# Optimization experiments

Hardware: AMD Instinct MI355X
Metric: run time of the kernel (lower is better)

Reference implementation:

```python
import jax, jax.numpy as jnp
import numpy as np

B, S, D_MODEL, HEAD = 4, 4096, 1024, 64


def rope(x):
    # Faithful to the torch code: 'odd' = even-indexed elems, 'even' = odd-indexed.
    b, s, d = x.shape
    half = d // 2
    pos = jnp.arange(s, dtype=x.dtype)
    theta = 1.0 / (10000.0 ** (jnp.arange(half, dtype=x.dtype) / half))
    freqs = pos[:, None] * theta[None, :]  # (s, half)
    sin, cos = jnp.sin(freqs), jnp.cos(freqs)
    odd = x[..., 0::2]
    even = x[..., 1::2]
    x_rot_even = even * cos + odd * sin
    x_rot_odd = odd * cos - even * sin
    return jnp.stack([x_rot_odd, x_rot_even], axis=-1).reshape(x.shape)


def setup_inputs() -> dict:
    key = jax.random.key(0)
    kx, kq, kk, kv = jax.random.split(key, 4)
    x = jax.random.normal(kx, (B, S, D_MODEL), dtype=jnp.float32)
    # torch Linear weights are [out,in]; we store the transposed [in,out] form.
    sc = 1.0 / np.sqrt(D_MODEL)
    Wq = jax.random.normal(kq, (D_MODEL, HEAD), dtype=jnp.float32) * sc
    Wk = jax.random.normal(kk, (D_MODEL, HEAD), dtype=jnp.float32) * sc
    Wv = jax.random.normal(kv, (D_MODEL, HEAD), dtype=jnp.float32) * sc
    return {"x": x, "Wq": Wq, "Wk": Wk, "Wv": Wv}


def reference(x, Wq, Wk, Wv):
    Q = rope(x @ Wq)  # (B, S, H)
    K = rope(x @ Wk)
    V = x @ Wv
    scale = K.shape[-1] ** -0.5
    scores = jnp.einsum('bqh,bkh->bqk', Q, K) * scale  # (B, S, S)
    causal = jnp.tril(jnp.ones((S, S), dtype=bool))
    scores = jnp.where(causal, scores, -jnp.inf)
    probs = jax.nn.softmax(scores, axis=-1)  # dropout p treated as 0 (eval)
    return jnp.einsum('bqk,bkh->bqh', probs, V)
```

## Files before the change

### kernel.cpp

```cpp
#include <hip/hip_runtime.h>
#include <stdint.h>


static constexpr int S_LEN  = 4096;
static constexpr int DMODEL = 1024;
static constexpr int NS     = 6;
static constexpr float SHIFT2  = 11.541560327111707f;
static constexpr float QSCALE  = 0.18033688011112042f;

typedef __attribute__((ext_vector_type(8))) short bf16x8;
typedef __attribute__((ext_vector_type(4))) float f32x4;

#define MFMA16(a, b, c) __builtin_amdgcn_mfma_f32_16x16x32_bf16((a), (b), (c), 0, 0, 0)

__device__ __forceinline__ unsigned short f2b(float f) {
    union { float f; unsigned int u; } v;
    v.f = f;
    unsigned int u = v.u;
    u += 0x7fffu + ((u >> 16) & 1u);
    return (unsigned short)(u >> 16);
}
__device__ __forceinline__ float b2f(unsigned short b) {
    union { unsigned int u; float f; } v;
    v.u = ((unsigned int)b) << 16;
    return v.f;
}

__device__ __forceinline__ float fast_exp2(float x) {
#if __has_builtin(__builtin_amdgcn_exp2f)
    return __builtin_amdgcn_exp2f(x);
#else
    return exp2f(x);
#endif
}

template <int CTRL>
__device__ __forceinline__ float dpp_f(float v) {
    return __builtin_bit_cast(float,
        __builtin_amdgcn_update_dpp(0, __builtin_bit_cast(int, v), CTRL, 0xf, 0xf, false));
}
__device__ __forceinline__ float rowsum16(float v) {
    v += dpp_f<0x128>(v);
    v += dpp_f<0x124>(v);
    v += dpp_f<0x122>(v);
    v += dpp_f<0x121>(v);
    return v;
}

__device__ __forceinline__ void dma16(const void* g, void* l) {
    __builtin_amdgcn_global_load_lds(
        (const __attribute__((address_space(1))) unsigned int*)g,
        (__attribute__((address_space(3))) unsigned int*)l, 16, 0, 0);
}

__global__ __launch_bounds__(256) void prep_wt(const float* __restrict__ Wq,
                                               const float* __restrict__ Wk,
                                               const float* __restrict__ Wv,
                                               unsigned short* __restrict__ Wt) {
    int idx = blockIdx.x * 256 + threadIdx.x;
    int c = idx >> 10;
    int k = idx & 1023;
    int mat = c >> 6, n = c & 63;
    const float* W = (mat == 0) ? Wq : (mat == 1) ? Wk : Wv;
    Wt[idx] = f2b(W[k * 64 + n]);
}

__global__ __launch_bounds__(256, 2) void proj_rope(const float* __restrict__ x,
                                                    const unsigned short* __restrict__ Wt,
                                                    unsigned short* __restrict__ Qg,
                                                    unsigned short* __restrict__ Kg,
                                                    unsigned short* __restrict__ Vtg) {
    __shared__ __align__(16) float          Xs[2][64 * 64];
    __shared__ __align__(16) unsigned short Bs[2][96 * 64];

    const int tid  = threadIdx.x;
    const int wave = tid >> 6, lane = tid & 63;
    const int l15  = lane & 15, quad = lane >> 4;
    const int bid  = blockIdx.x;
    const int wid  = (bid & 7) * 64 + (bid >> 3);
    const int rbase = (wid >> 1) * 64;
    const int ch    = wid & 1;

    f32x4 acc[6];
#pragma unroll
    for (int ft = 0; ft < 6; ++ft) acc[ft] = (f32x4){0.f, 0.f, 0.f, 0.f};

    const float* xg = x + (size_t)rbase * DMODEL;
    const unsigned short* wg = Wt + (size_t)(ch * 96) * 1024;

    auto stage = [&](int kc, int buf) {
#pragma unroll
        for (int ii = 0; ii < 4; ++ii) {
            const int i = 4 * wave + ii;
            const int row = i * 4 + (lane >> 4);
            const int gd = lane & 15;
            const int gs = (gd & 8) | ((gd & 7) ^ (row & 7));
            dma16(xg + (size_t)row * DMODEL + kc * 64 + gs * 4, &Xs[buf][i * 256]);
        }
#pragma unroll
        for (int jj = 0; jj < 3; ++jj) {
            const int j = 3 * wave + jj;
            const int col = j * 8 + (lane >> 3);
            const int gd = lane & 7;
            const int gs = gd ^ (col & 7);
            dma16(wg + (size_t)col * 1024 + kc * 64 + gs * 8, &Bs[buf][j * 512]);
        }
    };

    stage(0, 0);
    int p = 0;
    const int msk = l15 & 7;

#pragma unroll 1
    for (int kc = 0; kc < 16; ++kc) {
        __syncthreads();
        if (kc + 1 < 16) stage(kc + 1, p ^ 1);

        const float* Xb = &Xs[p][0];
        const unsigned short* Bb = &Bs[p][0];
        const int arow = wave * 16 + l15;

#pragma unroll
        for (int kk2 = 0; kk2 < 2; ++kk2) {
            float4 a0 = *reinterpret_cast<const float4*>(
                Xb + arow * 64 + (kk2 * 8 + ((quad * 2) ^ msk)) * 4);
            float4 a1 = *reinterpret_cast<const float4*>(
                Xb + arow * 64 + (kk2 * 8 + ((quad * 2 + 1) ^ msk)) * 4);
            bf16x8 af;
            af[0] = (short)f2b(a0.x); af[1] = (short)f2b(a0.y);
            af[2] = (short)f2b(a0.z); af[3] = (short)f2b(a0.w);
            af[4] = (short)f2b(a1.x); af[5] = (short)f2b(a1.y);
            af[6] = (short)f2b(a1.z); af[7] = (short)f2b(a1.w);
#pragma unroll
            for (int ft = 0; ft < 6; ++ft) {
                bf16x8 bf = *reinterpret_cast<const bf16x8*>(
                    Bb + (ft * 16 + l15) * 64 + ((kk2 * 4 + quad) ^ msk) * 8);
                acc[ft] = MFMA16(af, bf, acc[ft]);
            }
        }
        p ^= 1;
    }

#pragma unroll
    for (int ft = 0; ft < 6; ++ft) {
        const int col0 = ch * 96 + ft * 16;
        const int mat  = col0 >> 6;
        const int d    = (col0 & 63) + l15;
        if (mat < 2) {
            const int i = d >> 1;
            const float theta = exp2f((float)i * -0.41524101186f);
#pragma unroll
            for (int r = 0; r < 4; ++r) {
                const int gr   = rbase + wave * 16 + quad * 4 + r;
                const int spos = gr & (S_LEN - 1);
                float v = acc[ft][r];
                float partner = __shfl_xor(v, 1);
                float fr = (float)spos * theta;
                float sn = __sinf(fr);
                float cs = __cosf(fr);
                float outv = (d & 1) ? (v * cs + partner * sn)
                                     : (v * cs - partner * sn);
                if (mat == 0) outv *= QSCALE;
                unsigned short bv = f2b(outv);
                if (mat == 0) Qg[(size_t)gr * 64 + d] = bv;
                else          Kg[(size_t)gr * 64 + d] = bv;
            }
        } else {
            const int gr0  = rbase + wave * 16 + quad * 4;
            const int b    = gr0 >> 12;
            const int spos = gr0 & (S_LEN - 1);
            ushort4 vv;
            vv.x = f2b(acc[ft][0]);
            vv.y = f2b(acc[ft][1]);
            vv.z = f2b(acc[ft][2]);
            vv.w = f2b(acc[ft][3]);
            *reinterpret_cast<ushort4*>(
                &Vtg[(size_t)b * (64 * S_LEN) + (size_t)d * S_LEN + spos]) = vv;
        }
    }
}

__global__ __launch_bounds__(256) void attn_split(const unsigned short* __restrict__ Qg,
                                                  const unsigned short* __restrict__ Kg,
                                                  const unsigned short* __restrict__ Vtg,
                                                  unsigned short* __restrict__ OP,
                                                  float* __restrict__ L) {
    __shared__ __align__(16) unsigned short Klds[2][64 * 64];
    __shared__ __align__(16) unsigned short Vlds[2][64 * 64];
    __shared__ __align__(16) unsigned short Plds[4][16 * 72];

    const int tid  = threadIdx.x;
    const int wave = tid >> 6, lane = tid & 63;
    const int l15  = lane & 15, quad = lane >> 4;
    const int qt = 63 - blockIdx.x;
    const int split = blockIdx.y, b = blockIdx.z;
    const int qbase = qt * 64;

    const int total = qt + 1;
    const int chunk = (total + NS - 1) / NS;
    const int k0 = split * chunk;
    const int k1 = (k0 + chunk < total) ? (k0 + chunk) : total;

    bf16x8 qa[2];
    {
        const unsigned short* qrow = Qg + (size_t)(b * S_LEN + qbase + wave * 16 + l15) * 64;
        qa[0] = *reinterpret_cast<const bf16x8*>(qrow + quad * 8);
        qa[1] = *reinterpret_cast<const bf16x8*>(qrow + 32 + quad * 8);
    }

    f32x4 o[4];
    float lsum[4];
#pragma unroll
    for (int nt = 0; nt < 4; ++nt) o[nt] = (f32x4){0.f, 0.f, 0.f, 0.f};
#pragma unroll
    for (int r = 0; r < 4; ++r) lsum[r] = 0.f;

    const unsigned short* kgb = Kg  + (size_t)(b * S_LEN) * 64;
    const unsigned short* vgb = Vtg + (size_t)b * (64 * S_LEN);
    unsigned short* Pw = &Plds[wave][0];

    const int i0 = 2 * wave, i1 = 2 * wave + 1;
    const int r0 = (i0 * 64 + lane) >> 3, g0 = (i0 * 64 + lane) & 7;
    const int r1 = (i1 * 64 + lane) >> 3, g1 = (i1 * 64 + lane) & 7;
    const int sg0 = (g0 ^ (r0 & 7)) * 8, sg1 = (g1 ^ (r1 & 7)) * 8;

    auto stage = [&](int kt, int buf) {
        const unsigned short* kp = kgb + (size_t)kt * 64 * 64;
        dma16(kp + r0 * 64 + sg0, &Klds[buf][i0 * 512]);
        dma16(kp + r1 * 64 + sg1, &Klds[buf][i1 * 512]);
        const unsigned short* vp = vgb + (size_t)kt * 64;
        dma16(vp + (size_t)r0 * S_LEN + sg0, &Vlds[buf][i0 * 512]);
        dma16(vp + (size_t)r1 * S_LEN + sg1, &Vlds[buf][i1 * 512]);
    };

    if (k0 < k1) stage(k0, 0);

    int p = 0;
    for (int kt = k0; kt < k1; ++kt) {
        __syncthreads();
        if (kt + 1 < k1) stage(kt + 1, p ^ 1);

        const unsigned short* Kb = &Klds[p][0];
        const unsigned short* Vb = &Vlds[p][0];

        f32x4 s[4];
        __builtin_amdgcn_s_setprio(1);
#pragma unroll
        for (int nt = 0; nt < 4; ++nt) {
            const int rk = nt * 16 + l15;
            bf16x8 kb0 = *reinterpret_cast<const bf16x8*>(Kb + rk * 64 + ((quad ^ (rk & 7)) * 8));
            bf16x8 kb1 = *reinterpret_cast<const bf16x8*>(Kb + rk * 64 + (((4 + quad) ^ (rk & 7)) * 8));
            f32x4 z = (f32x4){0.f, 0.f, 0.f, 0.f};
            z = MFMA16(qa[0], kb0, z);
            z = MFMA16(qa[1], kb1, z);
            s[nt] = z;
        }
        __builtin_amdgcn_s_setprio(0);

        if (kt == qt) {
#pragma unroll
            for (int nt = 0; nt < 4; ++nt) {
                int key_l = nt * 16 + l15;
#pragma unroll
                for (int r = 0; r < 4; ++r) {
                    int q_l = wave * 16 + quad * 4 + r;
                    if (key_l > q_l) s[nt][r] = -1e30f;
                }
            }
        }

#pragma unroll
        for (int nt = 0; nt < 4; ++nt)
#pragma unroll
            for (int r = 0; r < 4; ++r) {
                float pv = fast_exp2(s[nt][r] - SHIFT2);
                s[nt][r] = pv;
                lsum[r] += pv;
            }

#pragma unroll
        for (int nt = 0; nt < 4; ++nt)
#pragma unroll
            for (int r = 0; r < 4; ++r)
                Pw[(quad * 4 + r) * 72 + nt * 16 + l15] = f2b(s[nt][r]);

        __builtin_amdgcn_s_setprio(1);
#pragma unroll
        for (int kc = 0; kc < 2; ++kc) {
            bf16x8 pa = *reinterpret_cast<const bf16x8*>(Pw + l15 * 72 + kc * 32 + quad * 8);
#pragma unroll
            for (int nt = 0; nt < 4; ++nt) {
                const int rv = nt * 16 + l15;
                bf16x8 vb = *reinterpret_cast<const bf16x8*>(
                    Vb + rv * 64 + (((kc * 4 + quad) ^ (rv & 7)) * 8));
                o[nt] = MFMA16(pa, vb, o[nt]);
            }
        }
        __builtin_amdgcn_s_setprio(0);
        p ^= 1;
    }

#pragma unroll
    for (int r = 0; r < 4; ++r) lsum[r] = rowsum16(lsum[r]);

    const size_t prow_base = ((size_t)(split * 4 + b)) * S_LEN;
#pragma unroll
    for (int nt = 0; nt < 4; ++nt)
#pragma unroll
        for (int r = 0; r < 4; ++r) {
            int row = qbase + wave * 16 + quad * 4 + r;
            OP[(prow_base + row) * 64 + nt * 16 + l15] = f2b(o[nt][r]);
        }
    if (l15 == 0) {
#pragma unroll
        for (int r = 0; r < 4; ++r) {
            int row = qbase + wave * 16 + quad * 4 + r;
            L[prow_base + row] = lsum[r];
        }
    }
}

__global__ __launch_bounds__(256) void combine(const unsigned short* __restrict__ OP,
                                               const float* __restrict__ L,
                                               float* __restrict__ out) {
    int idx = blockIdx.x * 256 + threadIdx.x;
    int dq  = idx & 15;
    int row = (idx >> 4) & (S_LEN - 1);
    int b   = idx >> 16;

    float num0 = 0.f, num1 = 0.f, num2 = 0.f, num3 = 0.f, den = 0.f;
#pragma unroll
    for (int s = 0; s < NS; ++s) {
        size_t pr = (size_t)(s * 4 + b) * S_LEN + row;
        den += L[pr];
        ushort4 v = *reinterpret_cast<const ushort4*>(OP + pr * 64 + dq * 4);
        num0 += b2f(v.x); num1 += b2f(v.y); num2 += b2f(v.z); num3 += b2f(v.w);
    }
    float inv = 1.f / den;
    float4 o = make_float4(num0 * inv, num1 * inv, num2 * inv, num3 * inv);
    *reinterpret_cast<float4*>(out + (size_t)idx * 4) = o;
}

extern "C" void kernel_launch(void* const* d_in, const int* in_sizes, int n_in,
                              void* d_out, int out_size, void* d_ws, size_t ws_size,
                              hipStream_t stream) {
    const float* x  = (const float*)d_in[0];
    const float* Wq = (const float*)d_in[1];
    const float* Wk = (const float*)d_in[2];
    const float* Wv = (const float*)d_in[3];
    float* out = (float*)d_out;

    unsigned char* base = (unsigned char*)d_ws;
    unsigned short* Qg  = (unsigned short*)(base);
    unsigned short* Kg  = (unsigned short*)(base + (2u << 20));
    unsigned short* Vtg = (unsigned short*)(base + (4u << 20));
    unsigned short* Wt  = (unsigned short*)(base + (6u << 20));
    float*          L   = (float*)(base + (6u << 20) + (1u << 19));
    unsigned short* OP  = (unsigned short*)(base + (7u << 20));

    prep_wt<<<768, 256, 0, stream>>>(Wq, Wk, Wv, Wt);
    proj_rope<<<512, 256, 0, stream>>>(x, Wt, Qg, Kg, Vtg);
    attn_split<<<dim3(64, NS, 4), 256, 0, stream>>>(Qg, Kg, Vtg, OP, L);
    combine<<<4096 / 4, 256, 0, stream>>>(OP, L, out);
}
```

Baseline: 151.3 us.

## Process two 64-row query subtiles per block to reuse staged K/V tiles

```diff
diff --git a/kernel.cpp b/kernel.cpp
--- a/kernel.cpp
+++ b/kernel.cpp
@@ -192,28 +192,33 @@
     const int tid  = threadIdx.x;
     const int wave = tid >> 6, lane = tid & 63;
     const int l15  = lane & 15, quad = lane >> 4;
-    const int qt = 63 - blockIdx.x;
+    const int qt128 = 31 - blockIdx.x;
     const int split = blockIdx.y, b = blockIdx.z;
-    const int qbase = qt * 64;
-
-    const int total = qt + 1;
+    const int qbase = qt128 * 128;
+
+    const int total = 2 * qt128 + 2;
     const int chunk = (total + NS - 1) / NS;
     const int k0 = split * chunk;
     const int k1 = (k0 + chunk < total) ? (k0 + chunk) : total;
 
-    bf16x8 qa[2];
-    {
-        const unsigned short* qrow = Qg + (size_t)(b * S_LEN + qbase + wave * 16 + l15) * 64;
-        qa[0] = *reinterpret_cast<const bf16x8*>(qrow + quad * 8);
-        qa[1] = *reinterpret_cast<const bf16x8*>(qrow + 32 + quad * 8);
-    }
-
-    f32x4 o[4];
-    float lsum[4];
-#pragma unroll
-    for (int nt = 0; nt < 4; ++nt) o[nt] = (f32x4){0.f, 0.f, 0.f, 0.f};
-#pragma unroll
-    for (int r = 0; r < 4; ++r) lsum[r] = 0.f;
+    bf16x8 qa[2][2];
+#pragma unroll
+    for (int st = 0; st < 2; ++st) {
+        const unsigned short* qrow =
+            Qg + (size_t)(b * S_LEN + qbase + st * 64 + wave * 16 + l15) * 64;
+        qa[st][0] = *reinterpret_cast<const bf16x8*>(qrow + quad * 8);
+        qa[st][1] = *reinterpret_cast<const bf16x8*>(qrow + 32 + quad * 8);
+    }
+
+    f32x4 o[2][4];
+    float lsum[2][4];
+#pragma unroll
+    for (int st = 0; st < 2; ++st)
+#pragma unroll
+        for (int nt = 0; nt < 4; ++nt) {
+            o[st][nt] = (f32x4){0.f, 0.f, 0.f, 0.f};
+            lsum[st][nt] = 0.f;
+        }
 
     const unsigned short* kgb = Kg  + (size_t)(b * S_LEN) * 64;
     const unsigned short* vgb = Vtg + (size_t)b * (64 * S_LEN);
@@ -243,79 +248,90 @@
         const unsigned short* Kb = &Klds[p][0];
         const unsigned short* Vb = &Vlds[p][0];
 
-        f32x4 s[4];
-        __builtin_amdgcn_s_setprio(1);
-#pragma unroll
-        for (int nt = 0; nt < 4; ++nt) {
-            const int rk = nt * 16 + l15;
-            bf16x8 kb0 = *reinterpret_cast<const bf16x8*>(Kb + rk * 64 + ((quad ^ (rk & 7)) * 8));
-            bf16x8 kb1 = *reinterpret_cast<const bf16x8*>(Kb + rk * 64 + (((4 + quad) ^ (rk & 7)) * 8));
-            f32x4 z = (f32x4){0.f, 0.f, 0.f, 0.f};
-            z = MFMA16(qa[0], kb0, z);
-            z = MFMA16(qa[1], kb1, z);
-            s[nt] = z;
-        }
-        __builtin_amdgcn_s_setprio(0);
-
-        if (kt == qt) {
+#pragma unroll
+        for (int st = 0; st < 2; ++st) {
+            const int lim = 2 * qt128 + st;
+            if (kt > lim) continue;
+
+            f32x4 s[4];
+            __builtin_amdgcn_s_setprio(1);
 #pragma unroll
             for (int nt = 0; nt < 4; ++nt) {
-                int key_l = nt * 16 + l15;
+                const int rk = nt * 16 + l15;
+                bf16x8 kb0 = *reinterpret_cast<const bf16x8*>(
+                    Kb + rk * 64 + ((quad ^ (rk & 7)) * 8));
+                bf16x8 kb1 = *reinterpret_cast<const bf16x8*>(
+                    Kb + rk * 64 + (((4 + quad) ^ (rk & 7)) * 8));
+                f32x4 z = (f32x4){0.f, 0.f, 0.f, 0.f};
+                z = MFMA16(qa[st][0], kb0, z);
+                z = MFMA16(qa[st][1], kb1, z);
+                s[nt] = z;
+            }
+            __builtin_amdgcn_s_setprio(0);
+
+            if (kt == lim) {
+#pragma unroll
+                for (int nt = 0; nt < 4; ++nt) {
+                    int key_l = nt * 16 + l15;
+#pragma unroll
+                    for (int r = 0; r < 4; ++r) {
+                        int q_l = wave * 16 + quad * 4 + r;
+                        if (key_l > q_l) s[nt][r] = -1e30f;
+                    }
+                }
+            }
+
+#pragma unroll
+            for (int nt = 0; nt < 4; ++nt)
 #pragma unroll
                 for (int r = 0; r < 4; ++r) {
-                    int q_l = wave * 16 + quad * 4 + r;
-                    if (key_l > q_l) s[nt][r] = -1e30f;
+                    float pv = fast_exp2(s[nt][r] - SHIFT2);
+                    s[nt][r] = pv;
+                    lsum[st][r] += pv;
                 }
-            }
-        }
-
+
+#pragma unroll
+            for (int nt = 0; nt < 4; ++nt)
+#pragma unroll
+                for (int r = 0; r < 4; ++r)
+                    Pw[(quad * 4 + r) * 72 + nt * 16 + l15] = f2b(s[nt][r]);
+
+            __builtin_amdgcn_s_setprio(1);
+#pragma unroll
+            for (int kc = 0; kc < 2; ++kc) {
+                bf16x8 pa = *reinterpret_cast<const bf16x8*>(
+                    Pw + l15 * 72 + kc * 32 + quad * 8);
+#pragma unroll
+                for (int nt = 0; nt < 4; ++nt) {
+                    const int rv = nt * 16 + l15;
+                    bf16x8 vb = *reinterpret_cast<const bf16x8*>(
+                        Vb + rv * 64 + (((kc * 4 + quad) ^ (rv & 7)) * 8));
+                    o[st][nt] = MFMA16(pa, vb, o[st][nt]);
+                }
+            }
+            __builtin_amdgcn_s_setprio(0);
+        }
+        p ^= 1;
+    }
+
+    const size_t prow_base = ((size_t)(split * 4 + b)) * S_LEN;
+#pragma unroll
+    for (int st = 0; st < 2; ++st) {
+#pragma unroll
+        for (int r = 0; r < 4; ++r) lsum[st][r] = rowsum16(lsum[st][r]);
 #pragma unroll
         for (int nt = 0; nt < 4; ++nt)
 #pragma unroll
             for (int r = 0; r < 4; ++r) {
-                float pv = fast_exp2(s[nt][r] - SHIFT2);
-                s[nt][r] = pv;
-                lsum[r] += pv;
-            }
-
-#pragma unroll
-        for (int nt = 0; nt < 4; ++nt)
-#pragma unroll
-            for (int r = 0; r < 4; ++r)
-                Pw[(quad * 4 + r) * 72 + nt * 16 + l15] = f2b(s[nt][r]);
-
-        __builtin_amdgcn_s_setprio(1);
-#pragma unroll
-        for (int kc = 0; kc < 2; ++kc) {
-            bf16x8 pa = *reinterpret_cast<const bf16x8*>(Pw + l15 * 72 + kc * 32 + quad * 8);
-#pragma unroll
-            for (int nt = 0; nt < 4; ++nt) {
-                const int rv = nt * 16 + l15;
-                bf16x8 vb = *reinterpret_cast<const bf16x8*>(
-                    Vb + rv * 64 + (((kc * 4 + quad) ^ (rv & 7)) * 8));
-                o[nt] = MFMA16(pa, vb, o[nt]);
-            }
-        }
-        __builtin_amdgcn_s_setprio(0);
-        p ^= 1;
-    }
-
-#pragma unroll
-    for (int r = 0; r < 4; ++r) lsum[r] = rowsum16(lsum[r]);
-
-    const size_t prow_base = ((size_t)(split * 4 + b)) * S_LEN;
-#pragma unroll
-    for (int nt = 0; nt < 4; ++nt)
-#pragma unroll
-        for (int r = 0; r < 4; ++r) {
-            int row = qbase + wave * 16 + quad * 4 + r;
-            OP[(prow_base + row) * 64 + nt * 16 + l15] = f2b(o[nt][r]);
-        }
-    if (l15 == 0) {
-#pragma unroll
-        for (int r = 0; r < 4; ++r) {
-            int row = qbase + wave * 16 + quad * 4 + r;
-            L[prow_base + row] = lsum[r];
+                int row = qbase + st * 64 + wave * 16 + quad * 4 + r;
+                OP[(prow_base + row) * 64 + nt * 16 + l15] = f2b(o[st][nt][r]);
+            }
+        if (l15 == 0) {
+#pragma unroll
+            for (int r = 0; r < 4; ++r) {
+                int row = qbase + st * 64 + wave * 16 + quad * 4 + r;
+                L[prow_base + row] = lsum[st][r];
+            }
         }
     }
 }
@@ -360,6 +376,6 @@
 
     prep_wt<<<768, 256, 0, stream>>>(Wq, Wk, Wv, Wt);
     proj_rope<<<512, 256, 0, stream>>>(x, Wt, Qg, Kg, Vtg);
-    attn_split<<<dim3(64, NS, 4), 256, 0, stream>>>(Qg, Kg, Vtg, OP, L);
+    attn_split<<<dim3(32, NS, 4), 256, 0, stream>>>(Qg, Kg, Vtg, OP, L);
     combine<<<4096 / 4, 256, 0, stream>>>(OP, L, out);
 }
```

Result: no change. 152.2 us (+0.6%).

## Fuse all stages into one cooperative persistent kernel with grid barriers

Applied to the files above, without the earlier changes.

```diff
diff --git a/kernel.cpp b/kernel.cpp
--- a/kernel.cpp
+++ b/kernel.cpp
@@ -5,6 +5,7 @@
 static constexpr int S_LEN  = 4096;
 static constexpr int DMODEL = 1024;
 static constexpr int NS     = 6;
+static constexpr int NBLK   = 512;
 static constexpr float SHIFT2  = 11.541560327111707f;
 static constexpr float QSCALE  = 0.18033688011112042f;
 
@@ -53,292 +54,317 @@
         (__attribute__((address_space(3))) unsigned int*)l, 16, 0, 0);
 }
 
-__global__ __launch_bounds__(256) void prep_wt(const float* __restrict__ Wq,
-                                               const float* __restrict__ Wk,
-                                               const float* __restrict__ Wv,
-                                               unsigned short* __restrict__ Wt) {
-    int idx = blockIdx.x * 256 + threadIdx.x;
-    int c = idx >> 10;
-    int k = idx & 1023;
-    int mat = c >> 6, n = c & 63;
-    const float* W = (mat == 0) ? Wq : (mat == 1) ? Wk : Wv;
-    Wt[idx] = f2b(W[k * 64 + n]);
-}
-
-__global__ __launch_bounds__(256, 2) void proj_rope(const float* __restrict__ x,
-                                                    const unsigned short* __restrict__ Wt,
-                                                    unsigned short* __restrict__ Qg,
-                                                    unsigned short* __restrict__ Kg,
-                                                    unsigned short* __restrict__ Vtg) {
-    __shared__ __align__(16) float          Xs[2][64 * 64];
-    __shared__ __align__(16) unsigned short Bs[2][96 * 64];
+__device__ __forceinline__ void gbar(unsigned int* c, unsigned int n) {
+    __syncthreads();
+    __threadfence();
+    if (threadIdx.x == 0) {
+        atomicAdd(c, 1u);
+        while (atomicAdd(c, 0u) < n) __builtin_amdgcn_s_sleep(2);
+    }
+    __syncthreads();
+    __threadfence();
+}
+
+__global__ __launch_bounds__(256, 2) void fused(
+    const float* __restrict__ x,  const float* __restrict__ Wq,
+    const float* __restrict__ Wk, const float* __restrict__ Wv,
+    unsigned short* __restrict__ Wt,
+    unsigned short* __restrict__ Qg, unsigned short* __restrict__ Kg,
+    unsigned short* __restrict__ Vtg,
+    unsigned short* __restrict__ OP, float* __restrict__ L,
+    float* __restrict__ out, unsigned int* __restrict__ syn) {
+    __shared__ __align__(16) unsigned char smem[57344];
+    __shared__ int s_id;
 
     const int tid  = threadIdx.x;
+    const int bid  = blockIdx.x;
     const int wave = tid >> 6, lane = tid & 63;
     const int l15  = lane & 15, quad = lane >> 4;
-    const int bid  = blockIdx.x;
-    const int wid  = (bid & 7) * 64 + (bid >> 3);
-    const int rbase = (wid >> 1) * 64;
-    const int ch    = wid & 1;
-
-    f32x4 acc[6];
-#pragma unroll
-    for (int ft = 0; ft < 6; ++ft) acc[ft] = (f32x4){0.f, 0.f, 0.f, 0.f};
-
-    const float* xg = x + (size_t)rbase * DMODEL;
-    const unsigned short* wg = Wt + (size_t)(ch * 96) * 1024;
-
-    auto stage = [&](int kc, int buf) {
-#pragma unroll
-        for (int ii = 0; ii < 4; ++ii) {
-            const int i = 4 * wave + ii;
-            const int row = i * 4 + (lane >> 4);
-            const int gd = lane & 15;
-            const int gs = (gd & 8) | ((gd & 7) ^ (row & 7));
-            dma16(xg + (size_t)row * DMODEL + kc * 64 + gs * 4, &Xs[buf][i * 256]);
+
+    for (int idx = bid * 256 + tid; idx < 192 * 1024; idx += NBLK * 256) {
+        int c = idx >> 10;
+        int k = idx & 1023;
+        int mat = c >> 6, n = c & 63;
+        const float* W = (mat == 0) ? Wq : (mat == 1) ? Wk : Wv;
+        Wt[idx] = f2b(W[k * 64 + n]);
+    }
+    gbar(syn + 0, NBLK);
+
+    {
+        float*          Xs = (float*)smem;
+        unsigned short* Bs = (unsigned short*)(smem + 32768);
+
+        const int wid   = (bid & 7) * 64 + (bid >> 3);
+        const int rbase = (wid >> 1) * 64;
+        const int ch    = wid & 1;
+
+        f32x4 acc[6];
+#pragma unroll
+        for (int ft = 0; ft < 6; ++ft) acc[ft] = (f32x4){0.f, 0.f, 0.f, 0.f};
+
+        const float* xg = x + (size_t)rbase * DMODEL;
+        const unsigned short* wg = Wt + (size_t)(ch * 96) * 1024;
+
+        auto stage = [&](int kc, int buf) {
+#pragma unroll
+            for (int ii = 0; ii < 4; ++ii) {
+                const int i = 4 * wave + ii;
+                const int row = i * 4 + (lane >> 4);
+                const int gd = lane & 15;
+                const int gs = (gd & 8) | ((gd & 7) ^ (row & 7));
+                dma16(xg + (size_t)row * DMODEL + kc * 64 + gs * 4,
+                      Xs + buf * 4096 + i * 256);
+            }
+#pragma unroll
+            for (int jj = 0; jj < 3; ++jj) {
+                const int j = 3 * wave + jj;
+                const int col = j * 8 + (lane >> 3);
+                const int gd = lane & 7;
+                const int gs = gd ^ (col & 7);
+                dma16(wg + (size_t)col * 1024 + kc * 64 + gs * 8,
+                      Bs + buf * 6144 + j * 512);
+            }
+        };
+
+        stage(0, 0);
+        int p = 0;
+        const int msk = l15 & 7;
+
+#pragma unroll 1
+        for (int kc = 0; kc < 16; ++kc) {
+            __syncthreads();
+            if (kc + 1 < 16) stage(kc + 1, p ^ 1);
+
+            const float* Xb = Xs + p * 4096;
+            const unsigned short* Bb = Bs + p * 6144;
+            const int arow = wave * 16 + l15;
+
+#pragma unroll
+            for (int kk2 = 0; kk2 < 2; ++kk2) {
+                float4 a0 = *reinterpret_cast<const float4*>(
+                    Xb + arow * 64 + (kk2 * 8 + ((quad * 2) ^ msk)) * 4);
+                float4 a1 = *reinterpret_cast<const float4*>(
+                    Xb + arow * 64 + (kk2 * 8 + ((quad * 2 + 1) ^ msk)) * 4);
+                bf16x8 af;
+                af[0] = (short)f2b(a0.x); af[1] = (short)f2b(a0.y);
+                af[2] = (short)f2b(a0.z); af[3] = (short)f2b(a0.w);
+                af[4] = (short)f2b(a1.x); af[5] = (short)f2b(a1.y);
+                af[6] = (short)f2b(a1.z); af[7] = (short)f2b(a1.w);
+#pragma unroll
+                for (int ft = 0; ft < 6; ++ft) {
+                    bf16x8 bf = *reinterpret_cast<const bf16x8*>(
+                        Bb + (ft * 16 + l15) * 64 + ((kk2 * 4 + quad) ^ msk) * 8);
+                    acc[ft] = MFMA16(af, bf, acc[ft]);
+                }
+            }
+            p ^= 1;
         }
-#pragma unroll
-        for (int jj = 0; jj < 3; ++jj) {
-            const int j = 3 * wave + jj;
-            const int col = j * 8 + (lane >> 3);
-            const int gd = lane & 7;
-            const int gs = gd ^ (col & 7);
-            dma16(wg + (size_t)col * 1024 + kc * 64 + gs * 8, &Bs[buf][j * 512]);
+
+#pragma unroll
+        for (int ft = 0; ft < 6; ++ft) {
+            const int col0 = ch * 96 + ft * 16;
+            const int mat  = col0 >> 6;
+            const int d    = (col0 & 63) + l15;
+            if (mat < 2) {
+                const int i = d >> 1;
+                const float theta = exp2f((float)i * -0.41524101186f);
+#pragma unroll
+                for (int r = 0; r < 4; ++r) {
+                    const int gr   = rbase + wave * 16 + quad * 4 + r;
+                    const int spos = gr & (S_LEN - 1);
+                    float v = acc[ft][r];
+                    float partner = __shfl_xor(v, 1);
+                    float fr = (float)spos * theta;
+                    float sn = __sinf(fr);
+                    float cs = __cosf(fr);
+                    float outv = (d & 1) ? (v * cs + partner * sn)
+                                         : (v * cs - partner * sn);
+                    if (mat == 0) outv *= QSCALE;
+                    unsigned short bv = f2b(outv);
+                    if (mat == 0) Qg[(size_t)gr * 64 + d] = bv;
+                    else          Kg[(size_t)gr * 64 + d] = bv;
+                }
+            } else {
+                const int gr0  = rbase + wave * 16 + quad * 4;
+                const int b    = gr0 >> 12;
+                const int spos = gr0 & (S_LEN - 1);
+                ushort4 vv;
+                vv.x = f2b(acc[ft][0]);
+                vv.y = f2b(acc[ft][1]);
+                vv.z = f2b(acc[ft][2]);
+                vv.w = f2b(acc[ft][3]);
+                *reinterpret_cast<ushort4*>(
+                    &Vtg[(size_t)b * (64 * S_LEN) + (size_t)d * S_LEN + spos]) = vv;
+            }
         }
-    };
-
-    stage(0, 0);
-    int p = 0;
-    const int msk = l15 & 7;
-
-#pragma unroll 1
-    for (int kc = 0; kc < 16; ++kc) {
-        __syncthreads();
-        if (kc + 1 < 16) stage(kc + 1, p ^ 1);
-
-        const float* Xb = &Xs[p][0];
-        const unsigned short* Bb = &Bs[p][0];
-        const int arow = wave * 16 + l15;
-
-#pragma unroll
-        for (int kk2 = 0; kk2 < 2; ++kk2) {
-            float4 a0 = *reinterpret_cast<const float4*>(
-                Xb + arow * 64 + (kk2 * 8 + ((quad * 2) ^ msk)) * 4);
-            float4 a1 = *reinterpret_cast<const float4*>(
-                Xb + arow * 64 + (kk2 * 8 + ((quad * 2 + 1) ^ msk)) * 4);
-            bf16x8 af;
-            af[0] = (short)f2b(a0.x); af[1] = (short)f2b(a0.y);
-            af[2] = (short)f2b(a0.z); af[3] = (short)f2b(a0.w);
-            af[4] = (short)f2b(a1.x); af[5] = (short)f2b(a1.y);
-            af[6] = (short)f2b(a1.z); af[7] = (short)f2b(a1.w);
-#pragma unroll
-            for (int ft = 0; ft < 6; ++ft) {
-                bf16x8 bf = *reinterpret_cast<const bf16x8*>(
-                    Bb + (ft * 16 + l15) * 64 + ((kk2 * 4 + quad) ^ msk) * 8);
-                acc[ft] = MFMA16(af, bf, acc[ft]);
-            }
+    }
+    gbar(syn + 1, NBLK);
+
+    {
+        unsigned short* Klds = (unsigned short*)smem;
+        unsigned short* Vlds = (unsigned short*)(smem + 16384);
+        unsigned short* Plds = (unsigned short*)(smem + 32768);
+        unsigned short* Pw   = Plds + wave * 1152;
+
+        const int i0 = 2 * wave, i1 = 2 * wave + 1;
+        const int r0 = (i0 * 64 + lane) >> 3, g0 = (i0 * 64 + lane) & 7;
+        const int r1 = (i1 * 64 + lane) >> 3, g1 = (i1 * 64 + lane) & 7;
+        const int sg0 = (g0 ^ (r0 & 7)) * 8, sg1 = (g1 ^ (r1 & 7)) * 8;
+
+        for (;;) {
+            if (tid == 0) s_id = (int)atomicAdd(syn + 3, 1u);
+            __syncthreads();
+            const int id = s_id;
+            if (id >= 64 * NS * 4) break;
+            const int qrow  = id / 24;
+            const int c24   = id - qrow * 24;
+            const int qt    = 63 - qrow;
+            const int split = c24 % 6;
+            const int b     = c24 / 6;
+            const int qbase = qt * 64;
+
+            const int total = qt + 1;
+            const int chunk = (total + NS - 1) / NS;
+            const int k0 = split * chunk;
+            const int k1 = (k0 + chunk < total) ? (k0 + chunk) : total;
+
+            bf16x8 qa[2];
+            {
+                const unsigned short* qrowp =
+                    Qg + (size_t)(b * S_LEN + qbase + wave * 16 + l15) * 64;
+                qa[0] = *reinterpret_cast<const bf16x8*>(qrowp + quad * 8);
+                qa[1] = *reinterpret_cast<const bf16x8*>(qrowp + 32 + quad * 8);
+            }
+
+            f32x4 o[4];
+            float lsum[4];
+#pragma unroll
+            for (int nt = 0; nt < 4; ++nt) o[nt] = (f32x4){0.f, 0.f, 0.f, 0.f};
+#pragma unroll
+            for (int r = 0; r < 4; ++r) lsum[r] = 0.f;
+
+            const unsigned short* kgb = Kg  + (size_t)(b * S_LEN) * 64;
+            const unsigned short* vgb = Vtg + (size_t)b * (64 * S_LEN);
+
+            auto stage = [&](int kt, int buf) {
+                const unsigned short* kp = kgb + (size_t)kt * 64 * 64;
+                dma16(kp + r0 * 64 + sg0, Klds + buf * 4096 + i0 * 512);
+                dma16(kp + r1 * 64 + sg1, Klds + buf * 4096 + i1 * 512);
+                const unsigned short* vp = vgb + (size_t)kt * 64;
+                dma16(vp + (size_t)r0 * S_LEN + sg0, Vlds + buf * 4096 + i0 * 512);
+                dma16(vp + (size_t)r1 * S_LEN + sg1, Vlds + buf * 4096 + i1 * 512);
+            };
+
+            if (k0 < k1) stage(k0, 0);
+
+            int p = 0;
+            for (int kt = k0; kt < k1; ++kt) {
+                __syncthreads();
+                if (kt + 1 < k1) stage(kt + 1, p ^ 1);
+
+                const unsigned short* Kb = Klds + p * 4096;
+                const unsigned short* Vb = Vlds + p * 4096;
+
+                f32x4 s[4];
+                __builtin_amdgcn_s_setprio(1);
+#pragma unroll
+                for (int nt = 0; nt < 4; ++nt) {
+                    const int rk = nt * 16 + l15;
+                    bf16x8 kb0 = *reinterpret_cast<const bf16x8*>(
+                        Kb + rk * 64 + ((quad ^ (rk & 7)) * 8));
+                    bf16x8 kb1 = *reinterpret_cast<const bf16x8*>(
+                        Kb + rk * 64 + (((4 + quad) ^ (rk & 7)) * 8));
+                    f32x4 z = (f32x4){0.f, 0.f, 0.f, 0.f};
+                    z = MFMA16(qa[0], kb0, z);
+                    z = MFMA16(qa[1], kb1, z);
+                    s[nt] = z;
+                }
+                __builtin_amdgcn_s_setprio(0);
+
+                if (kt == qt) {
+#pragma unroll
+                    for (int nt = 0; nt < 4; ++nt) {
+                        int key_l = nt * 16 + l15;
+#pragma unroll
+                        for (int r = 0; r < 4; ++r) {
+                            int q_l = wave * 16 + quad * 4 + r;
+                            if (key_l > q_l) s[nt][r] = -1e30f;
+                        }
+                    }
+                }
+
+#pragma unroll
+                for (int nt = 0; nt < 4; ++nt)
+#pragma unroll
+                    for (int r = 0; r < 4; ++r) {
+                        float pv = fast_exp2(s[nt][r] - SHIFT2);
+                        s[nt][r] = pv;
+                        lsum[r] += pv;
+                    }
+
+#pragma unroll
+                for (int nt = 0; nt < 4; ++nt)
+#pragma unroll
+                    for (int r = 0; r < 4; ++r)
+                        Pw[(quad * 4 + r) * 72 + nt * 16 + l15] = f2b(s[nt][r]);
+
+                __builtin_amdgcn_s_setprio(1);
+#pragma unroll
+                for (int kc = 0; kc < 2; ++kc) {
+                    bf16x8 pa = *reinterpret_cast<const bf16x8*>(
+                        Pw + l15 * 72 + kc * 32 + quad * 8);
+#pragma unroll
+                    for (int nt = 0; nt < 4; ++nt) {
+                        const int rv = nt * 16 + l15;
+                        bf16x8 vb = *reinterpret_cast<const bf16x8*>(
+                            Vb + rv * 64 + (((kc * 4 + quad) ^ (rv & 7)) * 8));
+                        o[nt] = MFMA16(pa, vb, o[nt]);
+                    }
+                }
+                __builtin_amdgcn_s_setprio(0);
+                p ^= 1;
+            }
+
+#pragma unroll
+            for (int r = 0; r < 4; ++r) lsum[r] = rowsum16(lsum[r]);
+
+            const size_t prow_base = ((size_t)(split * 4 + b)) * S_LEN;
+#pragma unroll
+            for (int nt = 0; nt < 4; ++nt)
+#pragma unroll
+                for (int r = 0; r < 4; ++r) {
+                    int row = qbase + wave * 16 + quad * 4 + r;
+                    OP[(prow_base + row) * 64 + nt * 16 + l15] = f2b(o[nt][r]);
+                }
+            if (l15 == 0) {
+#pragma unroll
+                for (int r = 0; r < 4; ++r) {
+                    int row = qbase + wave * 16 + quad * 4 + r;
+                    L[prow_base + row] = lsum[r];
+                }
+            }
+            __syncthreads();
         }
-        p ^= 1;
-    }
-
-#pragma unroll
-    for (int ft = 0; ft < 6; ++ft) {
-        const int col0 = ch * 96 + ft * 16;
-        const int mat  = col0 >> 6;
-        const int d    = (col0 & 63) + l15;
-        if (mat < 2) {
-            const int i = d >> 1;
-            const float theta = exp2f((float)i * -0.41524101186f);
-#pragma unroll
-            for (int r = 0; r < 4; ++r) {
-                const int gr   = rbase + wave * 16 + quad * 4 + r;
-                const int spos = gr & (S_LEN - 1);
-                float v = acc[ft][r];
-                float partner = __shfl_xor(v, 1);
-                float fr = (float)spos * theta;
-                float sn = __sinf(fr);
-                float cs = __cosf(fr);
-                float outv = (d & 1) ? (v * cs + partner * sn)
-                                     : (v * cs - partner * sn);
-                if (mat == 0) outv *= QSCALE;
-                unsigned short bv = f2b(outv);
-                if (mat == 0) Qg[(size_t)gr * 64 + d] = bv;
-                else          Kg[(size_t)gr * 64 + d] = bv;
-            }
-        } else {
-            const int gr0  = rbase + wave * 16 + quad * 4;
-            const int b    = gr0 >> 12;
-            const int spos = gr0 & (S_LEN - 1);
-            ushort4 vv;
-            vv.x = f2b(acc[ft][0]);
-            vv.y = f2b(acc[ft][1]);
-            vv.z = f2b(acc[ft][2]);
-            vv.w = f2b(acc[ft][3]);
-            *reinterpret_cast<ushort4*>(
-                &Vtg[(size_t)b * (64 * S_LEN) + (size_t)d * S_LEN + spos]) = vv;
+    }
+    gbar(syn + 2, NBLK);
+
+    for (int idx = bid * 256 + tid; idx < 262144; idx += NBLK * 256) {
+        int dq  = idx & 15;
+        int row = (idx >> 4) & (S_LEN - 1);
+        int b   = idx >> 16;
+
+        float num0 = 0.f, num1 = 0.f, num2 = 0.f, num3 = 0.f, den = 0.f;
+#pragma unroll
+        for (int s = 0; s < NS; ++s) {
+            size_t pr = (size_t)(s * 4 + b) * S_LEN + row;
+            den += L[pr];
+            ushort4 v = *reinterpret_cast<const ushort4*>(OP + pr * 64 + dq * 4);
+            num0 += b2f(v.x); num1 += b2f(v.y); num2 += b2f(v.z); num3 += b2f(v.w);
         }
-    }
-}
-
-__global__ __launch_bounds__(256) void attn_split(const unsigned short* __restrict__ Qg,
-                                                  const unsigned short* __restrict__ Kg,
-                                                  const unsigned short* __restrict__ Vtg,
-                                                  unsigned short* __restrict__ OP,
-                                                  float* __restrict__ L) {
-    __shared__ __align__(16) unsigned short Klds[2][64 * 64];
-    __shared__ __align__(16) unsigned short Vlds[2][64 * 64];
-    __shared__ __align__(16) unsigned short Plds[4][16 * 72];
-
-    const int tid  = threadIdx.x;
-    const int wave = tid >> 6, lane = tid & 63;
-    const int l15  = lane & 15, quad = lane >> 4;
-    const int qt = 63 - blockIdx.x;
-    const int split = blockIdx.y, b = blockIdx.z;
-    const int qbase = qt * 64;
-
-    const int total = qt + 1;
-    const int chunk = (total + NS - 1) / NS;
-    const int k0 = split * chunk;
-    const int k1 = (k0 + chunk < total) ? (k0 + chunk) : total;
-
-    bf16x8 qa[2];
-    {
-        const unsigned short* qrow = Qg + (size_t)(b * S_LEN + qbase + wave * 16 + l15) * 64;
-        qa[0] = *reinterpret_cast<const bf16x8*>(qrow + quad * 8);
-        qa[1] = *reinterpret_cast<const bf16x8*>(qrow + 32 + quad * 8);
-    }
-
-    f32x4 o[4];
-    float lsum[4];
-#pragma unroll
-    for (int nt = 0; nt < 4; ++nt) o[nt] = (f32x4){0.f, 0.f, 0.f, 0.f};
-#pragma unroll
-    for (int r = 0; r < 4; ++r) lsum[r] = 0.f;
-
-    const unsigned short* kgb = Kg  + (size_t)(b * S_LEN) * 64;
-    const unsigned short* vgb = Vtg + (size_t)b * (64 * S_LEN);
-    unsigned short* Pw = &Plds[wave][0];
-
-    const int i0 = 2 * wave, i1 = 2 * wave + 1;
-    const int r0 = (i0 * 64 + lane) >> 3, g0 = (i0 * 64 + lane) & 7;
-    const int r1 = (i1 * 64 + lane) >> 3, g1 = (i1 * 64 + lane) & 7;
-    const int sg0 = (g0 ^ (r0 & 7)) * 8, sg1 = (g1 ^ (r1 & 7)) * 8;
-
-    auto stage = [&](int kt, int buf) {
-        const unsigned short* kp = kgb + (size_t)kt * 64 * 64;
-        dma16(kp + r0 * 64 + sg0, &Klds[buf][i0 * 512]);
-        dma16(kp + r1 * 64 + sg1, &Klds[buf][i1 * 512]);
-        const unsigned short* vp = vgb + (size_t)kt * 64;
-        dma16(vp + (size_t)r0 * S_LEN + sg0, &Vlds[buf][i0 * 512]);
-        dma16(vp + (size_t)r1 * S_LEN + sg1, &Vlds[buf][i1 * 512]);
-    };
-
-    if (k0 < k1) stage(k0, 0);
-
-    int p = 0;
-    for (int kt = k0; kt < k1; ++kt) {
-        __syncthreads();
-        if (kt + 1 < k1) stage(kt + 1, p ^ 1);
-
-        const unsigned short* Kb = &Klds[p][0];
-        const unsigned short* Vb = &Vlds[p][0];
-
-        f32x4 s[4];
-        __builtin_amdgcn_s_setprio(1);
-#pragma unroll
-        for (int nt = 0; nt < 4; ++nt) {
-            const int rk = nt * 16 + l15;
-            bf16x8 kb0 = *reinterpret_cast<const bf16x8*>(Kb + rk * 64 + ((quad ^ (rk & 7)) * 8));
-            bf16x8 kb1 = *reinterpret_cast<const bf16x8*>(Kb + rk * 64 + (((4 + quad) ^ (rk & 7)) * 8));
-            f32x4 z = (f32x4){0.f, 0.f, 0.f, 0.f};
-            z = MFMA16(qa[0], kb0, z);
-            z = MFMA16(qa[1], kb1, z);
-            s[nt] = z;
-        }
-        __builtin_amdgcn_s_setprio(0);
-
-        if (kt == qt) {
-#pragma unroll
-            for (int nt = 0; nt < 4; ++nt) {
-                int key_l = nt * 16 + l15;
-#pragma unroll
-                for (int r = 0; r < 4; ++r) {
-                    int q_l = wave * 16 + quad * 4 + r;
-                    if (key_l > q_l) s[nt][r] = -1e30f;
-                }
-            }
-        }
-
-#pragma unroll
-        for (int nt = 0; nt < 4; ++nt)
-#pragma unroll
-            for (int r = 0; r < 4; ++r) {
-                float pv = fast_exp2(s[nt][r] - SHIFT2);
-                s[nt][r] = pv;
-                lsum[r] += pv;
-            }
-
-#pragma unroll
-        for (int nt = 0; nt < 4; ++nt)
-#pragma unroll
-            for (int r = 0; r < 4; ++r)
-                Pw[(quad * 4 + r) * 72 + nt * 16 + l15] = f2b(s[nt][r]);
-
-        __builtin_amdgcn_s_setprio(1);
-#pragma unroll
-        for (int kc = 0; kc < 2; ++kc) {
-            bf16x8 pa = *reinterpret_cast<const bf16x8*>(Pw + l15 * 72 + kc * 32 + quad * 8);
-#pragma unroll
-            for (int nt = 0; nt < 4; ++nt) {
-                const int rv = nt * 16 + l15;
-                bf16x8 vb = *reinterpret_cast<const bf16x8*>(
-                    Vb + rv * 64 + (((kc * 4 + quad) ^ (rv & 7)) * 8));
-                o[nt] = MFMA16(pa, vb, o[nt]);
-            }
-        }
-        __builtin_amdgcn_s_setprio(0);
-        p ^= 1;
-    }
-
-#pragma unroll
-    for (int r = 0; r < 4; ++r) lsum[r] = rowsum16(lsum[r]);
-
-    const size_t prow_base = ((size_t)(split * 4 + b)) * S_LEN;
-#pragma unroll
-    for (int nt = 0; nt < 4; ++nt)
-#pragma unroll
-        for (int r = 0; r < 4; ++r) {
-            int row = qbase + wave * 16 + quad * 4 + r;
-            OP[(prow_base + row) * 64 + nt * 16 + l15] = f2b(o[nt][r]);
-        }
-    if (l15 == 0) {
-#pragma unroll
-        for (int r = 0; r < 4; ++r) {
-            int row = qbase + wave * 16 + quad * 4 + r;
-            L[prow_base + row] = lsum[r];
-        }
-    }
-}
-
-__global__ __launch_bounds__(256) void combine(const unsigned short* __restrict__ OP,
-                                               const float* __restrict__ L,
-                                               float* __restrict__ out) {
-    int idx = blockIdx.x * 256 + threadIdx.x;
-    int dq  = idx & 15;
-    int row = (idx >> 4) & (S_LEN - 1);
-    int b   = idx >> 16;
-
-    float num0 = 0.f, num1 = 0.f, num2 = 0.f, num3 = 0.f, den = 0.f;
-#pragma unroll
-    for (int s = 0; s < NS; ++s) {
-        size_t pr = (size_t)(s * 4 + b) * S_LEN + row;
-        den += L[pr];
-        ushort4 v = *reinterpret_cast<const ushort4*>(OP + pr * 64 + dq * 4);
-        num0 += b2f(v.x); num1 += b2f(v.y); num2 += b2f(v.z); num3 += b2f(v.w);
-    }
-    float inv = 1.f / den;
-    float4 o = make_float4(num0 * inv, num1 * inv, num2 * inv, num3 * inv);
-    *reinterpret_cast<float4*>(out + (size_t)idx * 4) = o;
+        float inv = 1.f / den;
+        float4 ov = make_float4(num0 * inv, num1 * inv, num2 * inv, num3 * inv);
+        *reinterpret_cast<float4*>(out + (size_t)idx * 4) = ov;
+    }
 }
 
 extern "C" void kernel_launch(void* const* d_in, const int* in_sizes, int n_in,
@@ -351,15 +377,19 @@
     float* out = (float*)d_out;
 
     unsigned char* base = (unsigned char*)d_ws;
-    unsigned short* Qg  = (unsigned short*)(base);
-    unsigned short* Kg  = (unsigned short*)(base + (2u << 20));
-    unsigned short* Vtg = (unsigned short*)(base + (4u << 20));
-    unsigned short* Wt  = (unsigned short*)(base + (6u << 20));
-    float*          L   = (float*)(base + (6u << 20) + (1u << 19));
-    unsigned short* OP  = (unsigned short*)(base + (7u << 20));
-
-    prep_wt<<<768, 256, 0, stream>>>(Wq, Wk, Wv, Wt);
-    proj_rope<<<512, 256, 0, stream>>>(x, Wt, Qg, Kg, Vtg);
-    attn_split<<<dim3(64, NS, 4), 256, 0, stream>>>(Qg, Kg, Vtg, OP, L);
-    combine<<<4096 / 4, 256, 0, stream>>>(OP, L, out);
-}
+    unsigned short* Wt_p  = (unsigned short*)(base + (6u << 20));
+    unsigned short* Qg_p  = (unsigned short*)(base);
+    unsigned short* Kg_p  = (unsigned short*)(base + (2u << 20));
+    unsigned short* Vtg_p = (unsigned short*)(base + (4u << 20));
+    float*          L_p   = (float*)(base + (6u << 20) + (1u << 19));
+    unsigned short* OP_p  = (unsigned short*)(base + (7u << 20));
+    unsigned int*   syn_p = (unsigned int*)(base + (24u << 20));
+
+    hipMemsetAsync(syn_p, 0, 64, stream);
+
+    void* args[] = {(void*)&x, (void*)&Wq, (void*)&Wk, (void*)&Wv,
+                    (void*)&Wt_p, (void*)&Qg_p, (void*)&Kg_p, (void*)&Vtg_p,
+                    (void*)&OP_p, (void*)&L_p, (void*)&out, (void*)&syn_p};
+    hipLaunchCooperativeKernel((const void*)fused, dim3(NBLK), dim3(256),
+                               args, 0, stream);
+}
```

New measurement: 487.1 us. +222.0%, slower.
